# Performance work log

Hardware: AMD Instinct MI355X
Metric: run time of the kernel (lower is better)

The kernel has to match this reference:

```python
import jax, jax.numpy as jnp
import numpy as np

EPS = 1e-12


def _l2norm(x, axis):
    return x / jnp.maximum(jnp.linalg.norm(x, axis=axis, keepdims=True), EPS)


def _wn_weight(v, g):
    # weight norm over input axis (kernel_size=1): W = g * v / ||v||
    return g * v / jnp.maximum(jnp.linalg.norm(v, axis=0, keepdims=True), EPS)


def setup_inputs() -> dict:
    key = jax.random.key(0)
    ks = jax.random.split(key, 8)
    B, T, D = 16, 4096, 512
    N, K, d = 9, 1024, 8
    return {
        "z": jax.random.normal(ks[0], (B, T, D), dtype=jnp.float32),
        "in_v": jax.random.normal(ks[1], (N, D, d), dtype=jnp.float32) * 0.05,
        "in_g": jax.random.uniform(ks[2], (N, d), dtype=jnp.float32) + 0.5,
        "in_b": jax.random.normal(ks[3], (N, d), dtype=jnp.float32) * 0.01,
        "out_v": jax.random.normal(ks[4], (N, d, D), dtype=jnp.float32) * 0.05,
        "out_g": jax.random.uniform(ks[5], (N, D), dtype=jnp.float32) + 0.5,
        "out_b": jax.random.normal(ks[6], (N, D), dtype=jnp.float32) * 0.01,
        "codebooks": jax.random.normal(ks[7], (N, K, d), dtype=jnp.float32),
    }


def reference(z, in_v, in_g, in_b, out_v, out_g, out_b, codebooks):
    # Eval-mode ResidualVectorQuantize: n_quantizers = n_codebooks, mask all True.
    n_codebooks = codebooks.shape[0]
    residual = z
    z_q = jnp.zeros_like(z)
    commitment_loss = jnp.zeros((), z.dtype)
    codebook_loss = jnp.zeros((), z.dtype)
    codes, latents = [], []
    for i in range(n_codebooks):
        # in_proj (weight-normalized 1x1 conv == linear): [B,T,D] -> [B,T,d]
        W_in = _wn_weight(in_v[i], in_g[i])
        z_e = jnp.einsum("btd,dc->btc", residual, W_in) + in_b[i]
        # decode_latents: l2-normalize, pairwise sq-dist, nearest neighbor
        cb = codebooks[i]                      # [K, d] raw codebook
        enc_n = _l2norm(z_e, axis=-1)          # [B, T, d]
        cb_n = _l2norm(cb, axis=-1)            # [K, d]
        dist = (jnp.sum(enc_n * enc_n, -1, keepdims=True)
                - 2.0 * jnp.einsum("btc,kc->btk", enc_n, cb_n)
                + jnp.sum(cb_n * cb_n, -1))    # [B, T, K]
        indices = jnp.argmax(-dist, axis=-1)   # [B, T]
        z_q_i = cb[indices]                    # gather from raw codebook [B,T,d]
        # per-batch losses (mean over T, d)
        commit_i = jnp.mean((z_e - jax.lax.stop_gradient(z_q_i)) ** 2, axis=(1, 2))
        cbloss_i = jnp.mean((z_q_i - jax.lax.stop_gradient(z_e)) ** 2, axis=(1, 2))
        # straight-through estimator
        z_q_st = z_e + jax.lax.stop_gradient(z_q_i - z_e)
        # out_proj: [B,T,d] -> [B,T,D]
        W_out = _wn_weight(out_v[i], out_g[i])
        z_q_proj = jnp.einsum("btc,cd->btd", z_q_st, W_out) + out_b[i]
        z_q = z_q + z_q_proj
        residual = residual - z_q_proj
        commitment_loss = commitment_loss + commit_i.mean()
        codebook_loss = codebook_loss + cbloss_i.mean()
        codes.append(indices)
        latents.append(z_e)
    codes = jnp.stack(codes, axis=2)           # [B, T, N]
    latents = jnp.concatenate(latents, axis=2) # [B, T, N*d]
    return z_q, codes, latents, commitment_loss, codebook_loss
```

## Files before the change

### kernel.cpp

```cpp
#include <hip/hip_runtime.h>
#include <math.h>

#define ROWS   65536

#define WS_WPAD 0
#define WS_WOUT 49152
#define WS_CBT  86016
#define WS_SC   159744
#define WS_M    168960
#define WS_CACC 174144
#define WS_SOB  174216
#define WS_LOSS 174728

#define OUT_CODES 33554432
#define OUT_LAT   34144256
#define OUT_CLOSS 38862848
#define OUT_CBLOSS 38862849

__device__ __forceinline__ int pcol(int cc){ return (cc/9)*12 + (cc%9); }

__global__ __launch_bounds__(256) void prep1(const float* __restrict__ in_v,
    const float* __restrict__ in_g, const float* __restrict__ out_v,
    const float* __restrict__ out_g, const float* __restrict__ out_b,
    const float* __restrict__ cb, float* __restrict__ ws)
{
    int t = blockIdx.x*256 + threadIdx.x;
    if (t < 9216) {
        int i = t >> 10, k = t & 1023;
        const float* p = cb + (i*1024 + k)*8;
        float v[8]; float ssq = 0.f;
        #pragma unroll
        for (int c=0;c<8;c++){ v[c]=p[c]; ssq = fmaf(v[c],v[c],ssq); }
        float den = fmaxf(sqrtf(ssq), 1e-12f);
        float sc = 0.f;
        #pragma unroll
        for (int c=0;c<8;c++){ float cn = v[c]/den; ws[WS_CBT + (i*8+c)*1024 + k] = cn; sc = fmaf(cn,cn,sc); }
        ws[WS_SC + i*1024 + k] = sc;
    } else if (t < 13824) {
        int r = t - 9216; int j = r >> 9, tt = r & 511;
        float v[8]; float ssq = 0.f;
        #pragma unroll
        for (int a=0;a<8;a++){ v[a]=out_v[(j*8+a)*512+tt]; ssq=fmaf(v[a],v[a],ssq); }
        float den = fmaxf(sqrtf(ssq), 1e-12f);
        float g = out_g[j*512+tt];
        #pragma unroll
        for (int a=0;a<8;a++) ws[WS_WOUT + (j*8+a)*512 + tt] = g*v[a]/den;
    } else if (t < 18432) {
        int r = t - 13824;
        int w = r >> 6, l = r & 63;
        int i = w >> 3, c = w & 7;
        float v[8]; float ssq = 0.f;
        #pragma unroll
        for (int u=0;u<8;u++){ v[u] = in_v[(i*512 + l*8+u)*8 + c]; ssq = fmaf(v[u],v[u],ssq); }
        #pragma unroll
        for (int off=1; off<64; off<<=1) ssq += __shfl_xor(ssq, off, 64);
        float den = fmaxf(sqrtf(ssq), 1e-12f);
        float g = in_g[i*8+c];
        int pc = pcol(i*8+c);
        #pragma unroll
        for (int u=0;u<8;u++) ws[WS_WPAD + (l*8+u)*96 + pc] = g*v[u]/den;
    } else if (t < 18944) {
        int tt = t - 18432;
        float s = 0.f;
        for (int j=0;j<9;j++) s += out_b[j*512+tt];
        ws[WS_SOB + tt] = s;
    } else if (t == 18944) {
        *(double*)&ws[WS_LOSS] = 0.0;
    }
}

__global__ __launch_bounds__(256) void prep2(const float* __restrict__ out_b,
                                             float* __restrict__ ws)
{
    int g = blockIdx.x*256 + threadIdx.x;
    if (g < 41472) {
        int oi = g >> 3, part = g & 7;
        int j = oi / 576; int rem = oi % 576; int i = rem >> 6; int ab = rem & 63;
        int a = ab >> 3, b = ab & 7;
        int pc = pcol(i*8+b);
        const float* wo = ws + WS_WOUT + (j*8+a)*512 + part*64;
        const float* wp = ws + WS_WPAD + (part*64)*96 + pc;
        float s = 0.f;
        #pragma unroll
        for (int u=0; u<16; u++) {
            float4 w4 = *(const float4*)(wo + u*4);
            s = fmaf(w4.x, wp[(u*4+0)*96], s);
            s = fmaf(w4.y, wp[(u*4+1)*96], s);
            s = fmaf(w4.z, wp[(u*4+2)*96], s);
            s = fmaf(w4.w, wp[(u*4+3)*96], s);
        }
        #pragma unroll
        for (int off=1; off<8; off<<=1) s += __shfl_xor(s, off, 64);
        if (part == 0) ws[WS_M + oi] = s;
    } else if (g < 42048) {
        int r = g - 41472;
        int oi = r >> 3, part = r & 7;
        int i = oi >> 3, b = oi & 7;
        int pc = pcol(i*8+b);
        float s = 0.f;
        for (int u=0; u<64; u++) {
            int tt = part*64 + u;
            float bb = 0.f;
            for (int j=0;j<i;j++) bb += out_b[j*512+tt];
            s = fmaf(bb, ws[WS_WPAD + tt*96+pc], s);
        }
        #pragma unroll
        for (int off=1; off<8; off<<=1) s += __shfl_xor(s, off, 64);
        if (part == 0) ws[WS_CACC + oi] = s;
    }
}

__global__ __launch_bounds__(256) void gemm_in(const float* __restrict__ z,
    const float* __restrict__ in_b, const float* __restrict__ ws, float* __restrict__ out)
{
    __shared__ float AsT[32*132];
    __shared__ float Bs[32*96];
    int tid = threadIdx.x;
    int rowbase = blockIdx.x * 128;
    int tr = tid & 31, tc = tid >> 5;
    float acc[4][9];
    #pragma unroll
    for (int r=0;r<4;r++){
        #pragma unroll
        for(int c=0;c<9;c++) acc[r][c]=0.f;
    }
    int kq = tid & 7, rr = tid >> 3;
    for (int kk=0; kk<16; kk++) {
        #pragma unroll
        for (int p=0;p<4;p++){
            int row = rr + p*32;
            float4 a = *(const float4*)(z + (size_t)(rowbase+row)*512 + kk*32 + kq*4);
            AsT[(kq*4+0)*132 + row] = a.x;
            AsT[(kq*4+1)*132 + row] = a.y;
            AsT[(kq*4+2)*132 + row] = a.z;
            AsT[(kq*4+3)*132 + row] = a.w;
        }
        #pragma unroll
        for (int p=0;p<3;p++){
            int idx = p*256 + tid;
            *(float4*)(Bs + idx*4) = *(const float4*)(ws + WS_WPAD + kk*32*96 + idx*4);
        }
        __syncthreads();
        #pragma unroll 4
        for (int k=0;k<32;k++){
            float4 a  = *(const float4*)(AsT + k*132 + tr*4);
            float4 b0 = *(const float4*)(Bs + k*96 + tc*12);
            float4 b1 = *(const float4*)(Bs + k*96 + tc*12 + 4);
            float  b8 = Bs[k*96 + tc*12 + 8];
            float av[4] = {a.x,a.y,a.z,a.w};
            float bv[9] = {b0.x,b0.y,b0.z,b0.w,b1.x,b1.y,b1.z,b1.w,b8};
            #pragma unroll
            for (int r=0;r<4;r++){
                #pragma unroll
                for (int c=0;c<9;c++) acc[r][c] = fmaf(av[r], bv[c], acc[r][c]);
            }
        }
        __syncthreads();
    }
    #pragma unroll
    for (int c=0;c<9;c++){
        int cc = tc*9+c;
        float bias = in_b[cc];
        #pragma unroll
        for (int r=0;r<4;r++){
            int row = rowbase + tr*4 + r;
            out[OUT_LAT + (size_t)row*72 + cc] = acc[r][c] + bias;
        }
    }
}

__global__ __launch_bounds__(256, 2) void step_all(
    const float* __restrict__ cbooks, float* __restrict__ ws, float* __restrict__ out)
{
    __shared__ __align__(16) float zen_lds[4*32*12];
    __shared__ float codes_lds[128*13];
    __shared__ float warr[4];

    int tid = threadIdx.x;
    int w  = tid >> 6;
    int l  = tid & 63;
    int rowhalf = l >> 1;
    int ah = l & 1;
    int rowbase = blockIdx.x*128 + w*32;
    int kb = l*16;
    float* zen_w = zen_lds + w*384;

    float lacc = 0.f;

    float4 cbr[4][8];
    float4 hs4[4];

    #pragma unroll 1
    for (int i=0; i<9; i++){
        #pragma unroll
        for (int q=0;q<4;q++){
            #pragma unroll
            for (int c=0;c<8;c++)
                cbr[q][c] = *(const float4*)(ws + WS_CBT + i*8192 + c*1024 + kb + q*4);
            float4 s = *(const float4*)(ws + WS_SC + i*1024 + kb + q*4);
            hs4[q].x = s.x * -0.5f; hs4[q].y = s.y * -0.5f;
            hs4[q].z = s.z * -0.5f; hs4[q].w = s.w * -0.5f;
        }

        int row = rowbase + rowhalf;
        int rib = w*32 + rowhalf;
        float* lat = out + OUT_LAT + (size_t)row*72 + i*8;
        float4 p0 = *(const float4*)(lat);
        float4 p1 = *(const float4*)(lat+4);
        float ze[8] = {p0.x,p0.y,p0.z,p0.w,p1.x,p1.y,p1.z,p1.w};
        #pragma unroll
        for (int b=0;b<8;b++) ze[b] -= ws[WS_CACC + i*8 + b];
        #pragma unroll 1
        for (int j=0;j<i;j++){
            int kj = (int)codes_lds[rib*13 + j];
            const float* qp = cbooks + (size_t)(j*1024+kj)*8;
            float4 q0 = *(const float4*)(qp);
            float4 q1 = *(const float4*)(qp+4);
            float qa[8] = {q0.x,q0.y,q0.z,q0.w,q1.x,q1.y,q1.z,q1.w};
            const float* M = ws + WS_M + (j*9+i)*64;
            #pragma unroll
            for (int a=0;a<8;a++){
                #pragma unroll
                for (int b=0;b<8;b++) ze[b] = fmaf(-qa[a], M[a*8+b], ze[b]);
            }
        }
        float ssq = 0.f;
        #pragma unroll
        for (int c=0;c<8;c++) ssq = fmaf(ze[c],ze[c],ssq);
        float den = fmaxf(sqrtf(ssq), 1e-12f);
        float rden = 1.0f/den;
        float zen[8];
        #pragma unroll
        for (int c=0;c<8;c++) zen[c] = ze[c]*rden;
        if (ah == 0){
            float4 n0 = {zen[0],zen[1],zen[2],zen[3]};
            float4 n1 = {zen[4],zen[5],zen[6],zen[7]};
            *(float4*)(zen_w + rowhalf*12)     = n0;
            *(float4*)(zen_w + rowhalf*12 + 4) = n1;
        } else {
            float4 z0 = {ze[0],ze[1],ze[2],ze[3]};
            float4 z1 = {ze[4],ze[5],ze[6],ze[7]};
            *(float4*)(lat)   = z0;
            *(float4*)(lat+4) = z1;
        }

        int ksave = 0;
        #pragma unroll 2
        for (int rr=0; rr<32; rr++){
            float4 zv0 = *(const float4*)(zen_w + rr*12);
            float4 zv1 = *(const float4*)(zen_w + rr*12 + 4);
            float z[8] = {zv0.x,zv0.y,zv0.z,zv0.w,zv1.x,zv1.y,zv1.z,zv1.w};
            float bv = -3.0e38f; int rel = 0;
            #pragma unroll
            for (int q=0;q<4;q++){
                float d0 = hs4[q].x, d1 = hs4[q].y, d2 = hs4[q].z, d3 = hs4[q].w;
                #pragma unroll
                for (int c=0;c<8;c++){
                    d0 = fmaf(z[c], cbr[q][c].x, d0);
                    d1 = fmaf(z[c], cbr[q][c].y, d1);
                    d2 = fmaf(z[c], cbr[q][c].z, d2);
                    d3 = fmaf(z[c], cbr[q][c].w, d3);
                }
                bool c0 = d0 > bv; rel = c0 ? (q*4+0) : rel; bv = c0 ? d0 : bv;
                bool c1 = d1 > bv; rel = c1 ? (q*4+1) : rel; bv = c1 ? d1 : bv;
                bool c2 = d2 > bv; rel = c2 ? (q*4+2) : rel; bv = c2 ? d2 : bv;
                bool c3 = d3 > bv; rel = c3 ? (q*4+3) : rel; bv = c3 ? d3 : bv;
            }
            int kfull = kb + rel;
            float wm = bv;
            #pragma unroll
            for (int off=1; off<64; off<<=1) wm = fmaxf(wm, __shfl_xor(wm, off, 64));
            unsigned long long msk = __ballot(bv == wm);
            int ln = __ffsll((long long)msk) - 1;
            int kwin = __shfl(kfull, ln, 64);
            ksave = (rowhalf == rr) ? kwin : ksave;
        }

        if (ah == 0){
            const float* qp = cbooks + (size_t)(i*1024+ksave)*8;
            float4 q0 = *(const float4*)(qp);
            float4 q1 = *(const float4*)(qp+4);
            float e0 = ze[0]-q0.x, e1 = ze[1]-q0.y, e2 = ze[2]-q0.z, e3 = ze[3]-q0.w;
            float e4 = ze[4]-q1.x, e5 = ze[5]-q1.y, e6 = ze[6]-q1.z, e7 = ze[7]-q1.w;
            lacc = fmaf(e0,e0,lacc); lacc = fmaf(e1,e1,lacc);
            lacc = fmaf(e2,e2,lacc); lacc = fmaf(e3,e3,lacc);
            lacc = fmaf(e4,e4,lacc); lacc = fmaf(e5,e5,lacc);
            lacc = fmaf(e6,e6,lacc); lacc = fmaf(e7,e7,lacc);
        } else {
            out[OUT_CODES + (size_t)row*9 + i] = (float)ksave;
            codes_lds[rib*13 + i] = (float)ksave;
        }
    }

    #pragma unroll
    for (int off=1; off<64; off<<=1) lacc += __shfl_xor(lacc, off, 64);
    if ((tid & 63)==0) warr[tid>>6] = lacc;
    __syncthreads();
    if (tid==0){
        double bs = (double)warr[0]+(double)warr[1]+(double)warr[2]+(double)warr[3];
        atomicAdd((double*)&ws[WS_LOSS], bs);
    }
}

__global__ __launch_bounds__(256) void gemm_out(const float* __restrict__ cbooks,
    const float* __restrict__ ws, float* __restrict__ out)
{
    __shared__ float QLT[72*140];
    __shared__ float Ws[72*140];
    int tid = threadIdx.x;
    int rowbase = blockIdx.x*128;
    if (tid < 128){
        int row = rowbase + tid;
        int rsw = tid + (tid>>5)*4;
        for (int j=0;j<9;j++){
            int kj = (int)out[OUT_CODES + (size_t)row*9 + j];
            const float* qp = cbooks + (size_t)(j*1024+kj)*8;
            float4 q0 = *(const float4*)qp;
            float4 q1 = *(const float4*)(qp+4);
            QLT[(j*8+0)*140 + rsw] = q0.x;
            QLT[(j*8+1)*140 + rsw] = q0.y;
            QLT[(j*8+2)*140 + rsw] = q0.z;
            QLT[(j*8+3)*140 + rsw] = q0.w;
            QLT[(j*8+4)*140 + rsw] = q1.x;
            QLT[(j*8+5)*140 + rsw] = q1.y;
            QLT[(j*8+6)*140 + rsw] = q1.z;
            QLT[(j*8+7)*140 + rsw] = q1.w;
        }
    }
    int tc = tid & 15, tr = tid >> 4;
    int aoff = tr*8 + (tr>>2)*4;
    int boff = tc*8 + (tc>>2)*4;
    for (int cc=0; cc<4; cc++){
        __syncthreads();
        #pragma unroll
        for (int p=0;p<9;p++){
            int idx = p*256 + tid;
            int jr = idx >> 5; int cq = idx & 31;
            float4 wv = *(const float4*)(ws + WS_WOUT + jr*512 + cc*128 + cq*4);
            *(float4*)(Ws + jr*140 + cq*4 + (cq>>3)*4) = wv;
        }
        __syncthreads();
        float acc[8][8];
        #pragma unroll
        for (int r=0;r<8;r++){
            #pragma unroll
            for (int c=0;c<8;c++) acc[r][c]=0.f;
        }
        #pragma unroll 2
        for (int k=0;k<72;k++){
            float4 a0 = *(const float4*)(QLT + k*140 + aoff);
            float4 a1 = *(const float4*)(QLT + k*140 + aoff + 4);
            float4 b0 = *(const float4*)(Ws + k*140 + boff);
            float4 b1 = *(const float4*)(Ws + k*140 + boff + 4);
            float av[8] = {a0.x,a0.y,a0.z,a0.w,a1.x,a1.y,a1.z,a1.w};
            float bw[8] = {b0.x,b0.y,b0.z,b0.w,b1.x,b1.y,b1.z,b1.w};
            #pragma unroll
            for (int r=0;r<8;r++){
                #pragma unroll
                for (int c=0;c<8;c++) acc[r][c] = fmaf(av[r], bw[c], acc[r][c]);
            }
        }
        float4 s0 = *(const float4*)(ws + WS_SOB + cc*128 + tc*8);
        float4 s1 = *(const float4*)(ws + WS_SOB + cc*128 + tc*8 + 4);
        #pragma unroll
        for (int r=0;r<8;r++){
            int row = rowbase + tr*8 + r;
            float4 o0 = {acc[r][0]+s0.x, acc[r][1]+s0.y, acc[r][2]+s0.z, acc[r][3]+s0.w};
            float4 o1 = {acc[r][4]+s1.x, acc[r][5]+s1.y, acc[r][6]+s1.z, acc[r][7]+s1.w};
            *(float4*)(out + (size_t)row*512 + cc*128 + tc*8)     = o0;
            *(float4*)(out + (size_t)row*512 + cc*128 + tc*8 + 4) = o1;
        }
    }
    if (blockIdx.x==0 && tid==0){
        double L = *(const double*)(ws + WS_LOSS);
        float lv = (float)(L * (1.0/524288.0));
        out[OUT_CLOSS]  = lv;
        out[OUT_CBLOSS] = lv;
    }
}

extern "C" void kernel_launch(void* const* d_in, const int* in_sizes, int n_in,
                              void* d_out, int out_size, void* d_ws, size_t ws_size,
                              hipStream_t stream) {
    const float* z     = (const float*)d_in[0];
    const float* in_v  = (const float*)d_in[1];
    const float* in_g  = (const float*)d_in[2];
    const float* in_b  = (const float*)d_in[3];
    const float* out_v = (const float*)d_in[4];
    const float* out_g = (const float*)d_in[5];
    const float* out_b = (const float*)d_in[6];
    const float* cb    = (const float*)d_in[7];
    float* out = (float*)d_out;
    float* ws  = (float*)d_ws;

    prep1<<<75, 256, 0, stream>>>(in_v, in_g, out_v, out_g, out_b, cb, ws);
    prep2<<<165, 256, 0, stream>>>(out_b, ws);
    gemm_in<<<512, 256, 0, stream>>>(z, in_b, ws, out);
    step_all<<<512, 256, 0, stream>>>(cb, ws, out);
    gemm_out<<<512, 256, 0, stream>>>(cb, ws, out);
}
```

Before: 598.7 us.

## Fuse input GEMM, quantization steps, and output GEMM into one kernel

Merges gemm_in, step_all and gemm_out into a single per-128-row-block kernel. Projected latents stay in shared memory instead of being read back from global memory, and codes are taken from LDS for the output GEMM, which removes two kernel launches and some global round-trips. The shared-memory buffers are overlaid in one aliased array with repacked paddings, and a tiny finalize kernel now writes the losses. The risks are higher register and LDS pressure in the fused kernel, which may limit occupancy, and new bank-conflict patterns from the changed padding.

```diff
diff --git a/kernel.cpp b/kernel.cpp
--- a/kernel.cpp
+++ b/kernel.cpp
@@ -16,6 +16,14 @@
 #define OUT_LAT   34144256
 #define OUT_CLOSS 38862848
 #define OUT_CBLOSS 38862849
+
+#define SM_AST   0
+#define SM_BS    4224
+#define SM_P     0
+#define SM_QLT   0
+#define SM_REG2  9216
+#define SM_CODES 18720
+#define SM_WARR  19872
 
 __device__ __forceinline__ int pcol(int cc){ return (cc/9)*12 + (cc%9); }
 
@@ -110,83 +118,82 @@
     }
 }
 
-__global__ __launch_bounds__(256) void gemm_in(const float* __restrict__ z,
-    const float* __restrict__ in_b, const float* __restrict__ ws, float* __restrict__ out)
-{
-    __shared__ float AsT[32*132];
-    __shared__ float Bs[32*96];
-    int tid = threadIdx.x;
-    int rowbase = blockIdx.x * 128;
-    int tr = tid & 31, tc = tid >> 5;
-    float acc[4][9];
-    #pragma unroll
-    for (int r=0;r<4;r++){
-        #pragma unroll
-        for(int c=0;c<9;c++) acc[r][c]=0.f;
-    }
-    int kq = tid & 7, rr = tid >> 3;
-    for (int kk=0; kk<16; kk++) {
-        #pragma unroll
-        for (int p=0;p<4;p++){
-            int row = rr + p*32;
-            float4 a = *(const float4*)(z + (size_t)(rowbase+row)*512 + kk*32 + kq*4);
-            AsT[(kq*4+0)*132 + row] = a.x;
-            AsT[(kq*4+1)*132 + row] = a.y;
-            AsT[(kq*4+2)*132 + row] = a.z;
-            AsT[(kq*4+3)*132 + row] = a.w;
-        }
-        #pragma unroll
-        for (int p=0;p<3;p++){
-            int idx = p*256 + tid;
-            *(float4*)(Bs + idx*4) = *(const float4*)(ws + WS_WPAD + kk*32*96 + idx*4);
-        }
-        __syncthreads();
-        #pragma unroll 4
-        for (int k=0;k<32;k++){
-            float4 a  = *(const float4*)(AsT + k*132 + tr*4);
-            float4 b0 = *(const float4*)(Bs + k*96 + tc*12);
-            float4 b1 = *(const float4*)(Bs + k*96 + tc*12 + 4);
-            float  b8 = Bs[k*96 + tc*12 + 8];
-            float av[4] = {a.x,a.y,a.z,a.w};
-            float bv[9] = {b0.x,b0.y,b0.z,b0.w,b1.x,b1.y,b1.z,b1.w,b8};
-            #pragma unroll
-            for (int r=0;r<4;r++){
-                #pragma unroll
-                for (int c=0;c<9;c++) acc[r][c] = fmaf(av[r], bv[c], acc[r][c]);
-            }
-        }
-        __syncthreads();
-    }
-    #pragma unroll
-    for (int c=0;c<9;c++){
-        int cc = tc*9+c;
-        float bias = in_b[cc];
-        #pragma unroll
-        for (int r=0;r<4;r++){
-            int row = rowbase + tr*4 + r;
-            out[OUT_LAT + (size_t)row*72 + cc] = acc[r][c] + bias;
-        }
-    }
-}
-
-__global__ __launch_bounds__(256, 2) void step_all(
+__global__ __launch_bounds__(256, 2) void fused_all(
+    const float* __restrict__ z, const float* __restrict__ in_b,
     const float* __restrict__ cbooks, float* __restrict__ ws, float* __restrict__ out)
 {
-    __shared__ __align__(16) float zen_lds[4*32*12];
-    __shared__ float codes_lds[128*13];
-    __shared__ float warr[4];
-
+    __shared__ __align__(16) float smem[19880];
     int tid = threadIdx.x;
+    int brow = blockIdx.x * 128;
+
+    {
+        float* AsT = smem + SM_AST;
+        float* Bs  = smem + SM_BS;
+        int tr = tid & 31, tc = tid >> 5;
+        float acc[4][9];
+        #pragma unroll
+        for (int r=0;r<4;r++){
+            #pragma unroll
+            for(int c=0;c<9;c++) acc[r][c]=0.f;
+        }
+        int kq = tid & 7, rr = tid >> 3;
+        for (int kk=0; kk<16; kk++) {
+            #pragma unroll
+            for (int p=0;p<4;p++){
+                int row = rr + p*32;
+                float4 a = *(const float4*)(z + (size_t)(brow+row)*512 + kk*32 + kq*4);
+                AsT[(kq*4+0)*132 + row] = a.x;
+                AsT[(kq*4+1)*132 + row] = a.y;
+                AsT[(kq*4+2)*132 + row] = a.z;
+                AsT[(kq*4+3)*132 + row] = a.w;
+            }
+            #pragma unroll
+            for (int p=0;p<3;p++){
+                int idx = p*256 + tid;
+                *(float4*)(Bs + idx*4) = *(const float4*)(ws + WS_WPAD + kk*32*96 + idx*4);
+            }
+            __syncthreads();
+            #pragma unroll 4
+            for (int k=0;k<32;k++){
+                float4 a  = *(const float4*)(AsT + k*132 + tr*4);
+                float4 b0 = *(const float4*)(Bs + k*96 + tc*12);
+                float4 b1 = *(const float4*)(Bs + k*96 + tc*12 + 4);
+                float  b8 = Bs[k*96 + tc*12 + 8];
+                float av[4] = {a.x,a.y,a.z,a.w};
+                float bv[9] = {b0.x,b0.y,b0.z,b0.w,b1.x,b1.y,b1.z,b1.w,b8};
+                #pragma unroll
+                for (int r=0;r<4;r++){
+                    #pragma unroll
+                    for (int c=0;c<9;c++) acc[r][c] = fmaf(av[r], bv[c], acc[r][c]);
+                }
+            }
+            __syncthreads();
+        }
+        float* P = smem + SM_P;
+        #pragma unroll
+        for (int c=0;c<9;c++){
+            int cc = tc*9+c;
+            float bias = in_b[cc];
+            #pragma unroll
+            for (int r=0;r<4;r++){
+                int rl = tr*4 + r;
+                P[rl*72 + cc] = acc[r][c] + bias;
+            }
+        }
+        __syncthreads();
+    }
+
     int w  = tid >> 6;
     int l  = tid & 63;
     int rowhalf = l >> 1;
     int ah = l & 1;
-    int rowbase = blockIdx.x*128 + w*32;
+    int wrow = brow + w*32;
     int kb = l*16;
-    float* zen_w = zen_lds + w*384;
+    float* P = smem + SM_P;
+    float* zen_w = smem + SM_REG2 + w*384;
+    float* codes_lds = smem + SM_CODES;
 
     float lacc = 0.f;
-
     float4 cbr[4][8];
     float4 hs4[4];
 
@@ -202,17 +209,17 @@
             hs4[q].z = s.z * -0.5f; hs4[q].w = s.w * -0.5f;
         }
 
-        int row = rowbase + rowhalf;
+        int row = wrow + rowhalf;
         int rib = w*32 + rowhalf;
         float* lat = out + OUT_LAT + (size_t)row*72 + i*8;
-        float4 p0 = *(const float4*)(lat);
-        float4 p1 = *(const float4*)(lat+4);
+        float4 p0 = *(const float4*)(P + rib*72 + i*8);
+        float4 p1 = *(const float4*)(P + rib*72 + i*8 + 4);
         float ze[8] = {p0.x,p0.y,p0.z,p0.w,p1.x,p1.y,p1.z,p1.w};
         #pragma unroll
         for (int b=0;b<8;b++) ze[b] -= ws[WS_CACC + i*8 + b];
         #pragma unroll 1
         for (int j=0;j<i;j++){
-            int kj = (int)codes_lds[rib*13 + j];
+            int kj = (int)codes_lds[rib*9 + j];
             const float* qp = cbooks + (size_t)(j*1024+kj)*8;
             float4 q0 = *(const float4*)(qp);
             float4 q1 = *(const float4*)(qp+4);
@@ -249,17 +256,17 @@
         for (int rr=0; rr<32; rr++){
             float4 zv0 = *(const float4*)(zen_w + rr*12);
             float4 zv1 = *(const float4*)(zen_w + rr*12 + 4);
-            float z[8] = {zv0.x,zv0.y,zv0.z,zv0.w,zv1.x,zv1.y,zv1.z,zv1.w};
+            float zr[8] = {zv0.x,zv0.y,zv0.z,zv0.w,zv1.x,zv1.y,zv1.z,zv1.w};
             float bv = -3.0e38f; int rel = 0;
             #pragma unroll
             for (int q=0;q<4;q++){
                 float d0 = hs4[q].x, d1 = hs4[q].y, d2 = hs4[q].z, d3 = hs4[q].w;
                 #pragma unroll
                 for (int c=0;c<8;c++){
-                    d0 = fmaf(z[c], cbr[q][c].x, d0);
-                    d1 = fmaf(z[c], cbr[q][c].y, d1);
-                    d2 = fmaf(z[c], cbr[q][c].z, d2);
-                    d3 = fmaf(z[c], cbr[q][c].w, d3);
+                    d0 = fmaf(zr[c], cbr[q][c].x, d0);
+                    d1 = fmaf(zr[c], cbr[q][c].y, d1);
+                    d2 = fmaf(zr[c], cbr[q][c].z, d2);
+                    d3 = fmaf(zr[c], cbr[q][c].w, d3);
                 }
                 bool c0 = d0 > bv; rel = c0 ? (q*4+0) : rel; bv = c0 ? d0 : bv;
                 bool c1 = d1 > bv; rel = c1 ? (q*4+1) : rel; bv = c1 ? d1 : bv;
@@ -288,90 +295,92 @@
             lacc = fmaf(e6,e6,lacc); lacc = fmaf(e7,e7,lacc);
         } else {
             out[OUT_CODES + (size_t)row*9 + i] = (float)ksave;
-            codes_lds[rib*13 + i] = (float)ksave;
-        }
-    }
-
-    #pragma unroll
-    for (int off=1; off<64; off<<=1) lacc += __shfl_xor(lacc, off, 64);
-    if ((tid & 63)==0) warr[tid>>6] = lacc;
+            codes_lds[rib*9 + i] = (float)ksave;
+        }
+    }
+
+    {
+        float* warr = smem + SM_WARR;
+        #pragma unroll
+        for (int off=1; off<64; off<<=1) lacc += __shfl_xor(lacc, off, 64);
+        if ((tid & 63)==0) warr[w] = lacc;
+        __syncthreads();
+        if (tid==0){
+            double bs = (double)warr[0]+(double)warr[1]+(double)warr[2]+(double)warr[3];
+            atomicAdd((double*)&ws[WS_LOSS], bs);
+        }
+    }
+
     __syncthreads();
-    if (tid==0){
-        double bs = (double)warr[0]+(double)warr[1]+(double)warr[2]+(double)warr[3];
-        atomicAdd((double*)&ws[WS_LOSS], bs);
-    }
-}
-
-__global__ __launch_bounds__(256) void gemm_out(const float* __restrict__ cbooks,
-    const float* __restrict__ ws, float* __restrict__ out)
-{
-    __shared__ float QLT[72*140];
-    __shared__ float Ws[72*140];
-    int tid = threadIdx.x;
-    int rowbase = blockIdx.x*128;
-    if (tid < 128){
-        int row = rowbase + tid;
-        int rsw = tid + (tid>>5)*4;
-        for (int j=0;j<9;j++){
-            int kj = (int)out[OUT_CODES + (size_t)row*9 + j];
-            const float* qp = cbooks + (size_t)(j*1024+kj)*8;
-            float4 q0 = *(const float4*)qp;
-            float4 q1 = *(const float4*)(qp+4);
-            QLT[(j*8+0)*140 + rsw] = q0.x;
-            QLT[(j*8+1)*140 + rsw] = q0.y;
-            QLT[(j*8+2)*140 + rsw] = q0.z;
-            QLT[(j*8+3)*140 + rsw] = q0.w;
-            QLT[(j*8+4)*140 + rsw] = q1.x;
-            QLT[(j*8+5)*140 + rsw] = q1.y;
-            QLT[(j*8+6)*140 + rsw] = q1.z;
-            QLT[(j*8+7)*140 + rsw] = q1.w;
-        }
-    }
-    int tc = tid & 15, tr = tid >> 4;
-    int aoff = tr*8 + (tr>>2)*4;
-    int boff = tc*8 + (tc>>2)*4;
-    for (int cc=0; cc<4; cc++){
-        __syncthreads();
-        #pragma unroll
-        for (int p=0;p<9;p++){
-            int idx = p*256 + tid;
-            int jr = idx >> 5; int cq = idx & 31;
-            float4 wv = *(const float4*)(ws + WS_WOUT + jr*512 + cc*128 + cq*4);
-            *(float4*)(Ws + jr*140 + cq*4 + (cq>>3)*4) = wv;
-        }
-        __syncthreads();
-        float acc[8][8];
-        #pragma unroll
-        for (int r=0;r<8;r++){
-            #pragma unroll
-            for (int c=0;c<8;c++) acc[r][c]=0.f;
-        }
-        #pragma unroll 2
-        for (int k=0;k<72;k++){
-            float4 a0 = *(const float4*)(QLT + k*140 + aoff);
-            float4 a1 = *(const float4*)(QLT + k*140 + aoff + 4);
-            float4 b0 = *(const float4*)(Ws + k*140 + boff);
-            float4 b1 = *(const float4*)(Ws + k*140 + boff + 4);
-            float av[8] = {a0.x,a0.y,a0.z,a0.w,a1.x,a1.y,a1.z,a1.w};
-            float bw[8] = {b0.x,b0.y,b0.z,b0.w,b1.x,b1.y,b1.z,b1.w};
+    {
+        float* QLT = smem + SM_QLT;
+        float* Ws  = smem + SM_REG2;
+        if (tid < 128){
+            for (int j=0;j<9;j++){
+                int kj = (int)codes_lds[tid*9 + j];
+                const float* qp = cbooks + (size_t)(j*1024+kj)*8;
+                float4 q0 = *(const float4*)qp;
+                float4 q1 = *(const float4*)(qp+4);
+                QLT[(j*8+0)*128 + tid] = q0.x;
+                QLT[(j*8+1)*128 + tid] = q0.y;
+                QLT[(j*8+2)*128 + tid] = q0.z;
+                QLT[(j*8+3)*128 + tid] = q0.w;
+                QLT[(j*8+4)*128 + tid] = q1.x;
+                QLT[(j*8+5)*128 + tid] = q1.y;
+                QLT[(j*8+6)*128 + tid] = q1.z;
+                QLT[(j*8+7)*128 + tid] = q1.w;
+            }
+        }
+        int tc = tid & 15, tr = tid >> 4;
+        int aoff = tr*8;
+        int boff = tc*8 + (tc>>3)*4;
+        for (int cc=0; cc<4; cc++){
+            __syncthreads();
+            #pragma unroll
+            for (int p=0;p<9;p++){
+                int idx = p*256 + tid;
+                int jr = idx >> 5; int cq = idx & 31;
+                float4 wv = *(const float4*)(ws + WS_WOUT + jr*512 + cc*128 + cq*4);
+                *(float4*)(Ws + jr*132 + cq*4 + (cq>>4)*4) = wv;
+            }
+            __syncthreads();
+            float acc[8][8];
             #pragma unroll
             for (int r=0;r<8;r++){
                 #pragma unroll
-                for (int c=0;c<8;c++) acc[r][c] = fmaf(av[r], bw[c], acc[r][c]);
-            }
-        }
-        float4 s0 = *(const float4*)(ws + WS_SOB + cc*128 + tc*8);
-        float4 s1 = *(const float4*)(ws + WS_SOB + cc*128 + tc*8 + 4);
-        #pragma unroll
-        for (int r=0;r<8;r++){
-            int row = rowbase + tr*8 + r;
-            float4 o0 = {acc[r][0]+s0.x, acc[r][1]+s0.y, acc[r][2]+s0.z, acc[r][3]+s0.w};
-            float4 o1 = {acc[r][4]+s1.x, acc[r][5]+s1.y, acc[r][6]+s1.z, acc[r][7]+s1.w};
-            *(float4*)(out + (size_t)row*512 + cc*128 + tc*8)     = o0;
-            *(float4*)(out + (size_t)row*512 + cc*128 + tc*8 + 4) = o1;
-        }
-    }
-    if (blockIdx.x==0 && tid==0){
+                for (int c=0;c<8;c++) acc[r][c]=0.f;
+            }
+            #pragma unroll 2
+            for (int k=0;k<72;k++){
+                float4 a0 = *(const float4*)(QLT + k*128 + aoff);
+                float4 a1 = *(const float4*)(QLT + k*128 + aoff + 4);
+                float4 b0 = *(const float4*)(Ws + k*132 + boff);
+                float4 b1 = *(const float4*)(Ws + k*132 + boff + 4);
+                float av[8] = {a0.x,a0.y,a0.z,a0.w,a1.x,a1.y,a1.z,a1.w};
+                float bw[8] = {b0.x,b0.y,b0.z,b0.w,b1.x,b1.y,b1.z,b1.w};
+                #pragma unroll
+                for (int r=0;r<8;r++){
+                    #pragma unroll
+                    for (int c=0;c<8;c++) acc[r][c] = fmaf(av[r], bw[c], acc[r][c]);
+                }
+            }
+            float4 s0 = *(const float4*)(ws + WS_SOB + cc*128 + tc*8);
+            float4 s1 = *(const float4*)(ws + WS_SOB + cc*128 + tc*8 + 4);
+            #pragma unroll
+            for (int r=0;r<8;r++){
+                int row = brow + tr*8 + r;
+                float4 o0 = {acc[r][0]+s0.x, acc[r][1]+s0.y, acc[r][2]+s0.z, acc[r][3]+s0.w};
+                float4 o1 = {acc[r][4]+s1.x, acc[r][5]+s1.y, acc[r][6]+s1.z, acc[r][7]+s1.w};
+                *(float4*)(out + (size_t)row*512 + cc*128 + tc*8)     = o0;
+                *(float4*)(out + (size_t)row*512 + cc*128 + tc*8 + 4) = o1;
+            }
+        }
+    }
+}
+
+__global__ void finalize(const float* __restrict__ ws, float* __restrict__ out)
+{
+    if (threadIdx.x == 0){
         double L = *(const double*)(ws + WS_LOSS);
         float lv = (float)(L * (1.0/524288.0));
         out[OUT_CLOSS]  = lv;
@@ -395,7 +404,6 @@
 
     prep1<<<75, 256, 0, stream>>>(in_v, in_g, out_v, out_g, out_b, cb, ws);
     prep2<<<165, 256, 0, stream>>>(out_b, ws);
-    gemm_in<<<512, 256, 0, stream>>>(z, in_b, ws, out);
-    step_all<<<512, 256, 0, stream>>>(cb, ws, out);
-    gemm_out<<<512, 256, 0, stream>>>(cb, ws, out);
+    fused_all<<<512, 256, 0, stream>>>(z, in_b, cb, ws, out);
+    finalize<<<1, 64, 0, stream>>>(ws, out);
 }
```

Result: no change. 596.7 us (-0.3%).
